# Performance work log

Hardware: AMD Instinct MI355X
Metric: run time of the kernel (lower is better)

## Reference

```python
import jax, jax.numpy as jnp
import numpy as np
import math

EMB = 64
NEG_INF = -1e30

def _layernorm(x, g, b, eps=1e-5):
    mu = jnp.mean(x, axis=-1, keepdims=True)
    var = jnp.mean((x - mu) ** 2, axis=-1, keepdims=True)
    return (x - mu) * jax.lax.rsqrt(var + eps) * g + b

def setup_inputs() -> dict:
    key = jax.random.key(0)
    ks = jax.random.split(key, 8)
    b, t, n, d = 16, 12, 307, EMB
    s = 1.0 / math.sqrt(d)
    inp = {
        'x': jax.random.normal(ks[0], (b, t, n, d), dtype=jnp.float32),
        'stg': jax.random.uniform(ks[1], (b, n, t, n), dtype=jnp.float32),
        'topk': 3,
        'q_w': jax.random.normal(ks[2], (d, d), dtype=jnp.float32) * s,
        'q_b': jnp.zeros((d,), jnp.float32),
        'k_w': jax.random.normal(ks[3], (d, d), dtype=jnp.float32) * s,
        'k_b': jnp.zeros((d,), jnp.float32),
        'ln_g': jnp.ones((d,), jnp.float32),
        'ln_b': jnp.zeros((d,), jnp.float32),
        'ffn_ln_g': jnp.ones((d,), jnp.float32),
        'ffn_ln_b': jnp.zeros((d,), jnp.float32),
        'fc1_w': jax.random.normal(ks[4], (4 * d, d), dtype=jnp.float32) * s,
        'fc1_b': jnp.zeros((4 * d,), jnp.float32),
        'fc2_w': jax.random.normal(ks[5], (d, 4 * d), dtype=jnp.float32) * (0.5 * s),
        'fc2_b': jnp.zeros((d,), jnp.float32),
    }
    return inp

def reference(x, stg, topk, q_w, q_b, k_w, k_b, ln_g, ln_b, ffn_ln_g, ffn_ln_b, fc1_w, fc1_b, fc2_w, fc2_b):
    b, t, n, d = x.shape
    scale = 1.0 / math.sqrt(d)
    x_ = _layernorm(x, ln_g, ln_b)           # [b,t,n,d]
    y_ = x_[:, -1]                            # [b,n,d] last timestep
    q = y_ @ q_w.T + q_b                      # [b,n,d]
    k = x_ @ k_w.T + k_b                      # [b,t,n,d]
    dg = jnp.einsum('bnd,btmd->bntm', q, k) * scale
    sag = jax.nn.sigmoid(dg) * stg * scale    # gated scores [b,n,t,n]
    sag = sag.reshape(b, n, t * n)
    if topk > 0:
        kk = topk * n if topk < 5 else topk   # mirrors torch's self.topk *= n
        top_values, _ = jax.lax.top_k(sag, kk)
        thr = top_values[..., -1:]
        sag = jnp.where(sag > thr, sag, NEG_INF)  # strict >, as in torch code
    sag = jax.nn.softmax(sag, axis=-1).reshape(b, n, t, n)  # dropout in eval mode = identity
    o = jnp.einsum('bntm,btmd->bnd', sag, x_)
    h = o + y_
    # FFN: pre-norm residual MLP (LayerNorm -> Linear(d,4d) -> ReLU -> Linear(4d,d) + residual)
    z = _layernorm(h, ffn_ln_g, ffn_ln_b)
    z = jax.nn.relu(z @ fc1_w.T + fc1_b) @ fc2_w.T + fc2_b
    return h + z
```

## Files before the change

kernel.cpp:

```cpp
#include <hip/hip_runtime.h>

typedef __bf16 bf16x8 __attribute__((ext_vector_type(8)));
typedef float  f32x4  __attribute__((ext_vector_type(4)));
typedef unsigned short u16x8 __attribute__((ext_vector_type(8)));

constexpr int BB    = 16;
constexpr int TT    = 12;
constexpr int NN    = 307;
constexpr int TN    = TT * NN;
constexpr int ROWSX = BB * TT * NN;
constexpr int ROWSH = BB * NN;
constexpr int SST1  = 3712;
constexpr int SSTR  = 3840;
constexpr float SCALE = 0.125f;

__device__ __forceinline__ float wred_sum(float v) {
#pragma unroll
    for (int m = 32; m > 0; m >>= 1) v += __shfl_xor(v, m, 64);
    return v;
}

__global__ void fold_k(const float* __restrict__ qw, const float* __restrict__ qb,
                       const float* __restrict__ kw, const float* __restrict__ kb,
                       float* __restrict__ M, float* __restrict__ b2,
                       float* __restrict__ vv, float* __restrict__ cc) {
    int e = blockIdx.x, d = threadIdx.x;
    float acc = 0.f;
    for (int dp = 0; dp < 64; ++dp) acc += qw[dp * 64 + e] * kw[dp * 64 + d];
    M[e * 64 + d] = acc;
    float vp = wred_sum(qw[d * 64 + e] * kb[d]);
    if (d == 0) vv[e] = vp;
    if (e == 0) {
        float b = 0.f;
        for (int dp = 0; dp < 64; ++dp) b += qb[dp] * kw[dp * 64 + d];
        b2[d] = b;
        float cp = wred_sum(qb[d] * kb[d]);
        if (d == 0) *cc = cp;
    }
}

__global__ void wconv_k(const float* __restrict__ fc1w, const float* __restrict__ fc2w,
                        __bf16* __restrict__ fc1b16, __bf16* __restrict__ fc2b16) {
    int i = blockIdx.x * 256 + threadIdx.x;
    if (i < 16384) fc1b16[i] = (__bf16)fc1w[i];
    else fc2b16[i - 16384] = (__bf16)fc2w[i - 16384];
}

__global__ __launch_bounds__(256) void ln_k(const float* __restrict__ x,
                                            const float* __restrict__ g,
                                            const float* __restrict__ b,
                                            __bf16* __restrict__ xnb,
                                            float* __restrict__ y32) {
    int w = threadIdx.x >> 6, l = threadIdx.x & 63;
    int r = blockIdx.x * 4 + w;
    if (r >= ROWSX) return;
    float val = x[r * 64 + l];
    float mu  = wred_sum(val) * (1.f / 64.f);
    float dv  = val - mu;
    float var = wred_sum(dv * dv) * (1.f / 64.f);
    float xv  = dv * rsqrtf(var + 1e-5f) * g[l] + b[l];
    xnb[(size_t)r * 64 + l] = (__bf16)xv;
    int t = (r / NN) % TT;
    if (t == TT - 1) {
        int bbv = r / (NN * TT), n = r % NN;
        y32[(bbv * NN + n) * 64 + l] = xv;
    }
}

__global__ __launch_bounds__(256) void t_k(const __bf16* __restrict__ xnb,
                                           __bf16* __restrict__ xnT) {
    __shared__ unsigned short tile[64][65];
    int bb = blockIdx.y, j0 = blockIdx.x * 64, t = threadIdx.x;
    const unsigned short* src = (const unsigned short*)xnb;
    unsigned short* dst = (unsigned short*)xnT;
#pragma unroll
    for (int i = 0; i < 16; ++i) {
        int f = t + 256 * i, jr = f >> 6, dc = f & 63;
        int j = j0 + jr;
        tile[jr][dc] = (j < TN) ? src[((size_t)bb * TN + j) * 64 + dc] : (unsigned short)0;
    }
    __syncthreads();
#pragma unroll
    for (int i = 0; i < 16; ++i) {
        int f = t + 256 * i, d = f >> 6, jj = f & 63;
        dst[((size_t)bb * 64 + d) * SSTR + j0 + jj] = tile[jj][d];
    }
}

__global__ __launch_bounds__(256) void qt_k(const float* __restrict__ y32,
                                            const float* __restrict__ M,
                                            const float* __restrict__ b2,
                                            const float* __restrict__ vv,
                                            const float* __restrict__ ccp,
                                            __bf16* __restrict__ qtb,
                                            float* __restrict__ cq) {
    int w = threadIdx.x >> 6, l = threadIdx.x & 63;
    int rr = blockIdx.x * 4 + w;
    if (rr >= ROWSH) return;
    float y = y32[rr * 64 + l];
    float acc = b2[l];
#pragma unroll
    for (int e = 0; e < 64; ++e) acc += __shfl(y, e, 64) * M[e * 64 + l];
    qtb[(size_t)rr * 64 + l] = (__bf16)acc;
    float cp = wred_sum(y * vv[l]);
    if (l == 0) cq[rr] = cp + *ccp;
}

__global__ __launch_bounds__(256) void score_k(const __bf16* __restrict__ qtb,
                                               const float* __restrict__ cq,
                                               const __bf16* __restrict__ xnb,
                                               const float* __restrict__ stg,
                                               __bf16* __restrict__ sag) {
    __shared__ float sstg[64 * 132];
    int bb = blockIdx.z, n0 = blockIdx.y * 64, j0 = blockIdx.x * 128;
    int t = threadIdx.x;
    int w = t >> 6, lane = t & 63;
    int m16 = lane & 15, q4 = lane >> 4;

#pragma unroll
    for (int i = 0; i < 8; ++i) {
        int flat = t + i * 256;
        int row = flat >> 5, c4 = (flat & 31) * 4;
        int n = n0 + row;
        float4 v = {0.f, 0.f, 0.f, 0.f};
        if (n < NN) {
            size_t rb = (size_t)(bb * NN + n) * TN;
            int j = j0 + c4;
            if (j + 3 < TN) v = *(const float4*)(stg + rb + j);
            else {
                if (j + 0 < TN) v.x = stg[rb + j + 0];
                if (j + 1 < TN) v.y = stg[rb + j + 1];
                if (j + 2 < TN) v.z = stg[rb + j + 2];
                if (j + 3 < TN) v.w = stg[rb + j + 3];
            }
        }
        *(float4*)&sstg[row * 132 + c4] = v;
    }

    const bf16x8* ap = (const bf16x8*)(qtb + ((size_t)bb * NN + n0 + w * 16 + m16) * 64);
    bf16x8 a0 = ap[q4], a1 = ap[q4 + 4];
    f32x4 acc[8];
#pragma unroll
    for (int jt = 0; jt < 8; ++jt) {
        const bf16x8* bp = (const bf16x8*)(xnb + ((size_t)bb * TN + j0 + jt * 16 + m16) * 64);
        bf16x8 b0 = bp[q4], b1 = bp[q4 + 4];
        f32x4 c = {0.f, 0.f, 0.f, 0.f};
        c = __builtin_amdgcn_mfma_f32_16x16x32_bf16(a0, b0, c, 0, 0, 0);
        c = __builtin_amdgcn_mfma_f32_16x16x32_bf16(a1, b1, c, 0, 0, 0);
        acc[jt] = c;
    }
    int nbase = n0 + w * 16 + q4 * 4;
    float cn[4];
#pragma unroll
    for (int r = 0; r < 4; ++r) {
        int n = nbase + r;
        cn[r] = (n < NN) ? cq[bb * NN + n] : 0.f;
    }
    __syncthreads();

    u16x8 wvr[4];
#pragma unroll
    for (int r = 0; r < 4; ++r) {
        int nloc = w * 16 + q4 * 4 + r;
#pragma unroll
        for (int jt = 0; jt < 8; ++jt) {
            int j = j0 + jt * 16 + m16;
            float sv = sstg[nloc * 132 + jt * 16 + m16];
            float dg = (acc[jt][r] + cn[r]) * SCALE;
            float s  = 1.f / (1.f + __expf(-dg));
            float wv = (j < TN) ? s * sv * SCALE : 0.f;
            __bf16 wb16 = (__bf16)wv;
            wvr[r][jt] = *(unsigned short*)&wb16;
        }
    }
    __syncthreads();

    unsigned short* wb = (unsigned short*)sstg;
#pragma unroll
    for (int r = 0; r < 4; ++r) {
        int nloc = w * 16 + q4 * 4 + r;
#pragma unroll
        for (int jt = 0; jt < 8; ++jt)
            wb[nloc * 136 + jt * 16 + m16] = wvr[r][jt];
    }
    __syncthreads();

#pragma unroll
    for (int i = 0; i < 4; ++i) {
        int chunk = t + i * 256;
        int row = chunk >> 4, c8 = (chunk & 15) * 8;
        int n = n0 + row;
        if (n < NN) {
            u16x8 v = *(const u16x8*)&wb[row * 136 + c8];
            *(u16x8*)((unsigned short*)sag + (size_t)(bb * NN + n) * SST1 + j0 + c8) = v;
        }
    }
}

__global__ __launch_bounds__(512) void attn_k(const __bf16* __restrict__ sagB,
                                              const __bf16* __restrict__ xnT,
                                              const float* __restrict__ y32,
                                              const int* __restrict__ topk_p,
                                              float* __restrict__ h) {
    __shared__ unsigned short sg[8][3720];
    __shared__ float red[4][8][16];
    int t = threadIdx.x;
    int bb = blockIdx.y, n0 = blockIdx.x * 8;
    int wid = t >> 6, lane = t & 63;
    int m16 = lane & 15, q4 = lane >> 4;

    int topkv = *topk_p;
    bool selAll = (topkv <= 0);
    int kk = 0;
    if (!selAll) {
        kk = (topkv < 5) ? topkv * NN : topkv;
        if (kk > TN) kk = TN;
    }

    int n = n0 + wid;
    const u16x8* src = (const u16x8*)((const unsigned short*)sagB +
                                      (size_t)(bb * NN + min(n, NN - 1)) * SST1);
    u16x8 va[8];
#pragma unroll
    for (int ci = 0; ci < 8; ++ci) {
        int c = lane + (ci << 6);
        u16x8 v = {0, 0, 0, 0, 0, 0, 0, 0};
        if (c < 464) v = src[c];
        va[ci] = v;
    }
    int vmb = 0;
#pragma unroll
    for (int ci = 0; ci < 8; ++ci)
#pragma unroll
        for (int e = 0; e < 8; ++e) vmb = max(vmb, (int)va[ci][e]);
#pragma unroll
    for (int m = 32; m > 0; m >>= 1) vmb = max(vmb, __shfl_xor(vmb, m, 64));
    float vmax = __uint_as_float(((unsigned)vmb) << 16);

    unsigned thrb = 0;
    if (!selAll) {
        unsigned lo = 0, hi = (unsigned)vmb;
        while (lo < hi) {
            unsigned mid = (lo + hi) >> 1;
            int cnt = 0;
#pragma unroll
            for (int ci = 0; ci < 8; ++ci)
#pragma unroll
                for (int e = 0; e < 8; ++e)
                    cnt += (int)__popcll(__ballot((unsigned)va[ci][e] > mid));
            if (cnt < kk) hi = mid; else lo = mid + 1;
        }
        thrb = lo;
    }

    float local = 0.f;
#pragma unroll
    for (int ci = 0; ci < 8; ++ci) {
        int c = lane + (ci << 6);
        int nvv = (c < 460) ? 8 : ((c == 460) ? 4 : 0);
#pragma unroll
        for (int e = 0; e < 8; ++e) {
            unsigned u = va[ci][e];
            bool sel = selAll ? (e < nvv) : (u > thrb);
            float ev = sel ? __expf(__uint_as_float(u << 16) - vmax) : 0.f;
            local += ev;
            __bf16 eb = (__bf16)ev;
            va[ci][e] = *(unsigned short*)&eb;
        }
    }
    local = wred_sum(local);
    bool uni = !(local > 0.f);
    float inv = uni ? 0.f : 1.f / local;
    float uval = 1.f / (float)TN;
#pragma unroll
    for (int ci = 0; ci < 8; ++ci) {
        int c = lane + (ci << 6);
        if (c < 464) {
            int nvv = (c < 460) ? 8 : ((c == 460) ? 4 : 0);
            bf16x8 o;
#pragma unroll
            for (int e = 0; e < 8; ++e) {
                if (uni) o[e] = (e < nvv) ? (__bf16)uval : (__bf16)0.f;
                else {
                    unsigned short us = va[ci][e];
                    float ev = (float)(*(__bf16*)&us);
                    o[e] = (__bf16)(ev * inv);
                }
            }
            *(bf16x8*)&sg[wid][c * 8] = o;
        }
    }
    __syncthreads();

    int dg = wid & 3, kh = wid >> 2;
    bf16x8 zf;
#pragma unroll
    for (int e = 0; e < 8; ++e) zf[e] = (__bf16)0.f;
    f32x4 acc0 = {0.f, 0.f, 0.f, 0.f}, acc1 = {0.f, 0.f, 0.f, 0.f};
    const __bf16* bbase = xnT + ((size_t)bb * 64 + dg * 16 + m16) * SSTR + q4 * 8;
    int kbeg = kh * 1856;
    for (int ks = 0; ks < 58; ks += 2) {
        int k0 = kbeg + ks * 32, k1 = k0 + 32;
        bf16x8 a0 = (m16 < 8) ? *(const bf16x8*)&sg[m16][k0 + q4 * 8] : zf;
        bf16x8 a1 = (m16 < 8) ? *(const bf16x8*)&sg[m16][k1 + q4 * 8] : zf;
        bf16x8 b0 = *(const bf16x8*)(bbase + k0);
        bf16x8 b1 = *(const bf16x8*)(bbase + k1);
        acc0 = __builtin_amdgcn_mfma_f32_16x16x32_bf16(a0, b0, acc0, 0, 0, 0);
        acc1 = __builtin_amdgcn_mfma_f32_16x16x32_bf16(a1, b1, acc1, 0, 0, 0);
    }
    if (kh == 0) {
        if (q4 < 2) {
#pragma unroll
            for (int r = 0; r < 4; ++r)
                red[dg][q4 * 4 + r][m16] = acc0[r] + acc1[r];
        }
    }
    __syncthreads();
    if (kh == 1 && q4 < 2) {
#pragma unroll
        for (int r = 0; r < 4; ++r) {
            int row = q4 * 4 + r;
            int nn2 = n0 + row;
            if (nn2 < NN) {
                size_t o = (size_t)(bb * NN + nn2) * 64 + dg * 16 + m16;
                h[o] = acc0[r] + acc1[r] + red[dg][row][m16] + y32[o];
            }
        }
    }
}

__global__ __launch_bounds__(256) void ffn_k(const float* __restrict__ h,
                                             const float* __restrict__ g,
                                             const float* __restrict__ bln,
                                             const __bf16* __restrict__ fc1b16,
                                             const float* __restrict__ fc1b,
                                             const __bf16* __restrict__ fc2b16,
                                             const float* __restrict__ fc2b,
                                             float* __restrict__ out) {
    __shared__ __bf16 zb[16 * 68];
    __shared__ __bf16 ab[16 * 264];
    int t = threadIdx.x, r0 = blockIdx.x * 16;
    int wid = t >> 6, lane = t & 63;
    int m16 = lane & 15, q4 = lane >> 4;

#pragma unroll
    for (int q = 0; q < 4; ++q) {
        int rl = wid * 4 + q;
        float val = h[(size_t)(r0 + rl) * 64 + lane];
        float mu  = wred_sum(val) * (1.f / 64.f);
        float dv  = val - mu;
        float var = wred_sum(dv * dv) * (1.f / 64.f);
        zb[rl * 68 + lane] = (__bf16)(dv * rsqrtf(var + 1e-5f) * g[lane] + bln[lane]);
    }
    __syncthreads();

    bf16x8 a0 = *(const bf16x8*)&zb[m16 * 68 + q4 * 8];
    bf16x8 a1 = *(const bf16x8*)&zb[m16 * 68 + 32 + q4 * 8];
#pragma unroll
    for (int jt2 = 0; jt2 < 4; ++jt2) {
        int j0t = (wid * 4 + jt2) * 16;
        const __bf16* bp = fc1b16 + (size_t)(j0t + m16) * 64 + q4 * 8;
        f32x4 c = {0.f, 0.f, 0.f, 0.f};
        c = __builtin_amdgcn_mfma_f32_16x16x32_bf16(a0, *(const bf16x8*)bp, c, 0, 0, 0);
        c = __builtin_amdgcn_mfma_f32_16x16x32_bf16(a1, *(const bf16x8*)(bp + 32), c, 0, 0, 0);
        int j = j0t + m16;
        float bias = fc1b[j];
#pragma unroll
        for (int r = 0; r < 4; ++r)
            ab[(q4 * 4 + r) * 264 + j] = (__bf16)fmaxf(c[r] + bias, 0.f);
    }
    __syncthreads();

    f32x4 c2a = {0.f, 0.f, 0.f, 0.f}, c2b = {0.f, 0.f, 0.f, 0.f};
    const __bf16* b2p = fc2b16 + (size_t)(wid * 16 + m16) * 256 + q4 * 8;
#pragma unroll
    for (int k8 = 0; k8 < 8; k8 += 2) {
        bf16x8 aa0 = *(const bf16x8*)&ab[m16 * 264 + k8 * 32 + q4 * 8];
        bf16x8 aa1 = *(const bf16x8*)&ab[m16 * 264 + (k8 + 1) * 32 + q4 * 8];
        c2a = __builtin_amdgcn_mfma_f32_16x16x32_bf16(aa0, *(const bf16x8*)(b2p + k8 * 32), c2a, 0, 0, 0);
        c2b = __builtin_amdgcn_mfma_f32_16x16x32_bf16(aa1, *(const bf16x8*)(b2p + (k8 + 1) * 32), c2b, 0, 0, 0);
    }
    int d = wid * 16 + m16;
    float bias2 = fc2b[d];
#pragma unroll
    for (int r = 0; r < 4; ++r) {
        size_t row = (size_t)(r0 + q4 * 4 + r);
        out[row * 64 + d] = h[row * 64 + d] + c2a[r] + c2b[r] + bias2;
    }
}

extern "C" void kernel_launch(void* const* d_in, const int* in_sizes, int n_in,
                              void* d_out, int out_size, void* d_ws, size_t ws_size,
                              hipStream_t stream) {
    const float* x    = (const float*)d_in[0];
    const float* stg  = (const float*)d_in[1];
    const int*   topk = (const int*)d_in[2];
    const float* qw   = (const float*)d_in[3];
    const float* qb   = (const float*)d_in[4];
    const float* kw   = (const float*)d_in[5];
    const float* kb   = (const float*)d_in[6];
    const float* lng  = (const float*)d_in[7];
    const float* lnb  = (const float*)d_in[8];
    const float* flng = (const float*)d_in[9];
    const float* flnb = (const float*)d_in[10];
    const float* fc1w = (const float*)d_in[11];
    const float* fc1b = (const float*)d_in[12];
    const float* fc2w = (const float*)d_in[13];
    const float* fc2b = (const float*)d_in[14];
    float* out = (float*)d_out;

    float* ws = (float*)d_ws;
    __bf16* xnb = (__bf16*)ws;
    float* p1   = ws + 1886208;
    __bf16* xnT = (__bf16*)p1;
    float* p2   = p1 + 1966080;
    __bf16* qtb = (__bf16*)p2;
    float* y32  = p2 + 157696;
    float* cq   = y32 + 314368;
    float* M    = cq + 4928;
    float* b2   = M + 4096;
    float* vv   = b2 + 64;
    float* cc   = vv + 64;
    __bf16* fc1b16 = (__bf16*)(cc + 16);
    __bf16* fc2b16 = (__bf16*)((float*)fc1b16 + 8192);
    __bf16* sag = (__bf16*)((float*)fc2b16 + 8192);
    float* h    = (float*)sag + 9116672;

    fold_k<<<64, 64, 0, stream>>>(qw, qb, kw, kb, M, b2, vv, cc);
    wconv_k<<<128, 256, 0, stream>>>(fc1w, fc2w, fc1b16, fc2b16);
    ln_k<<<(ROWSX + 3) / 4, 256, 0, stream>>>(x, lng, lnb, xnb, y32);
    t_k<<<dim3((TN + 63) / 64, BB), 256, 0, stream>>>(xnb, xnT);
    qt_k<<<(ROWSH + 3) / 4, 256, 0, stream>>>(y32, M, b2, vv, cc, qtb, cq);
    score_k<<<dim3((TN + 127) / 128, (NN + 63) / 64, BB), 256, 0, stream>>>(qtb, cq, xnb, stg, sag);
    attn_k<<<dim3((NN + 7) / 8, BB), 512, 0, stream>>>(sag, xnT, y32, topk, h);
    ffn_k<<<ROWSH / 16, 256, 0, stream>>>(h, flng, flnb, fc1b16, fc1b, fc2b16, fc2b, out);
}
```

Baseline: 273.6 us.

## Process two attention rows per wave in attn_k with interleaved top-k searches

```diff
diff --git a/kernel.cpp b/kernel.cpp
--- a/kernel.cpp
+++ b/kernel.cpp
@@ -197,15 +197,15 @@
     }
 }
 
-__global__ __launch_bounds__(512) void attn_k(const __bf16* __restrict__ sagB,
-                                              const __bf16* __restrict__ xnT,
-                                              const float* __restrict__ y32,
-                                              const int* __restrict__ topk_p,
-                                              float* __restrict__ h) {
+__global__ __launch_bounds__(512, 4) void attn_k(const __bf16* __restrict__ sagB,
+                                                 const __bf16* __restrict__ xnT,
+                                                 const float* __restrict__ y32,
+                                                 const int* __restrict__ topk_p,
+                                                 float* __restrict__ h) {
     __shared__ unsigned short sg[8][3720];
     __shared__ float red[4][8][16];
     int t = threadIdx.x;
-    int bb = blockIdx.y, n0 = blockIdx.x * 8;
+    int bb = blockIdx.y, n0 = blockIdx.x * 16;
     int wid = t >> 6, lane = t & 63;
     int m16 = lane & 15, q4 = lane >> 4;
 
@@ -217,116 +217,143 @@
         if (kk > TN) kk = TN;
     }
 
-    int n = n0 + wid;
-    const u16x8* src = (const u16x8*)((const unsigned short*)sagB +
-                                      (size_t)(bb * NN + min(n, NN - 1)) * SST1);
-    u16x8 va[8];
+    int nA = n0 + wid, nB = n0 + 8 + wid;
+    const u16x8* srcA = (const u16x8*)((const unsigned short*)sagB +
+                                       (size_t)(bb * NN + min(nA, NN - 1)) * SST1);
+    const u16x8* srcB = (const u16x8*)((const unsigned short*)sagB +
+                                       (size_t)(bb * NN + min(nB, NN - 1)) * SST1);
+    u16x8 va[8], vb[8];
 #pragma unroll
     for (int ci = 0; ci < 8; ++ci) {
         int c = lane + (ci << 6);
-        u16x8 v = {0, 0, 0, 0, 0, 0, 0, 0};
-        if (c < 464) v = src[c];
-        va[ci] = v;
-    }
-    int vmb = 0;
+        u16x8 v0 = {0, 0, 0, 0, 0, 0, 0, 0}, v1 = v0;
+        if (c < 464) { v0 = srcA[ci * 64 + lane]; v1 = srcB[ci * 64 + lane]; }
+        va[ci] = v0; vb[ci] = v1;
+    }
+
+    int vmA = 0, vmB = 0;
 #pragma unroll
     for (int ci = 0; ci < 8; ++ci)
 #pragma unroll
-        for (int e = 0; e < 8; ++e) vmb = max(vmb, (int)va[ci][e]);
-#pragma unroll
-    for (int m = 32; m > 0; m >>= 1) vmb = max(vmb, __shfl_xor(vmb, m, 64));
-    float vmax = __uint_as_float(((unsigned)vmb) << 16);
-
-    unsigned thrb = 0;
+        for (int e = 0; e < 8; ++e) {
+            vmA = max(vmA, (int)va[ci][e]);
+            vmB = max(vmB, (int)vb[ci][e]);
+        }
+#pragma unroll
+    for (int m = 32; m > 0; m >>= 1) {
+        vmA = max(vmA, __shfl_xor(vmA, m, 64));
+        vmB = max(vmB, __shfl_xor(vmB, m, 64));
+    }
+    float vmaxA = __uint_as_float(((unsigned)vmA) << 16);
+    float vmaxB = __uint_as_float(((unsigned)vmB) << 16);
+
+    unsigned thrA = 0, thrB = 0;
     if (!selAll) {
-        unsigned lo = 0, hi = (unsigned)vmb;
-        while (lo < hi) {
-            unsigned mid = (lo + hi) >> 1;
-            int cnt = 0;
+        unsigned loA = 0, hiA = (unsigned)vmA;
+        unsigned loB = 0, hiB = (unsigned)vmB;
+        while (loA < hiA || loB < hiB) {
+            bool doA = loA < hiA, doB = loB < hiB;
+            unsigned midA = (loA + hiA) >> 1, midB = (loB + hiB) >> 1;
+            int cntA = 0, cntB = 0;
 #pragma unroll
             for (int ci = 0; ci < 8; ++ci)
 #pragma unroll
-                for (int e = 0; e < 8; ++e)
-                    cnt += (int)__popcll(__ballot((unsigned)va[ci][e] > mid));
-            if (cnt < kk) hi = mid; else lo = mid + 1;
+                for (int e = 0; e < 8; ++e) {
+                    if (doA) cntA += (int)__popcll(__ballot((unsigned)va[ci][e] > midA));
+                    if (doB) cntB += (int)__popcll(__ballot((unsigned)vb[ci][e] > midB));
+                }
+            if (doA) { if (cntA < kk) hiA = midA; else loA = midA + 1; }
+            if (doB) { if (cntB < kk) hiB = midB; else loB = midB + 1; }
         }
-        thrb = lo;
-    }
-
-    float local = 0.f;
-#pragma unroll
-    for (int ci = 0; ci < 8; ++ci) {
-        int c = lane + (ci << 6);
-        int nvv = (c < 460) ? 8 : ((c == 460) ? 4 : 0);
-#pragma unroll
-        for (int e = 0; e < 8; ++e) {
-            unsigned u = va[ci][e];
-            bool sel = selAll ? (e < nvv) : (u > thrb);
-            float ev = sel ? __expf(__uint_as_float(u << 16) - vmax) : 0.f;
-            local += ev;
-            __bf16 eb = (__bf16)ev;
-            va[ci][e] = *(unsigned short*)&eb;
-        }
-    }
-    local = wred_sum(local);
-    bool uni = !(local > 0.f);
-    float inv = uni ? 0.f : 1.f / local;
-    float uval = 1.f / (float)TN;
-#pragma unroll
-    for (int ci = 0; ci < 8; ++ci) {
-        int c = lane + (ci << 6);
-        if (c < 464) {
-            int nvv = (c < 460) ? 8 : ((c == 460) ? 4 : 0);
-            bf16x8 o;
-#pragma unroll
-            for (int e = 0; e < 8; ++e) {
-                if (uni) o[e] = (e < nvv) ? (__bf16)uval : (__bf16)0.f;
-                else {
-                    unsigned short us = va[ci][e];
-                    float ev = (float)(*(__bf16*)&us);
-                    o[e] = (__bf16)(ev * inv);
-                }
-            }
-            *(bf16x8*)&sg[wid][c * 8] = o;
-        }
-    }
-    __syncthreads();
+        thrA = loA; thrB = loB;
+    }
+
+#define SOFTMAX_ROW(VV, THR, VMX)                                                \
+    {                                                                            \
+        float local = 0.f;                                                       \
+        _Pragma("unroll") for (int ci = 0; ci < 8; ++ci) {                       \
+            int c = lane + (ci << 6);                                            \
+            int nvv = (c < 460) ? 8 : ((c == 460) ? 4 : 0);                      \
+            _Pragma("unroll") for (int e = 0; e < 8; ++e) {                      \
+                unsigned u = VV[ci][e];                                          \
+                bool sel = selAll ? (e < nvv) : (u > THR);                       \
+                float ev = sel ? __expf(__uint_as_float(u << 16) - VMX) : 0.f;   \
+                local += ev;                                                     \
+                __bf16 eb = (__bf16)ev;                                          \
+                VV[ci][e] = *(unsigned short*)&eb;                               \
+            }                                                                    \
+        }                                                                        \
+        local = wred_sum(local);                                                 \
+        bool uni = !(local > 0.f);                                               \
+        float inv = uni ? 0.f : 1.f / local;                                     \
+        float uval = 1.f / (float)TN;                                            \
+        _Pragma("unroll") for (int ci = 0; ci < 8; ++ci) {                       \
+            int c = lane + (ci << 6);                                            \
+            int nvv = (c < 460) ? 8 : ((c == 460) ? 4 : 0);                      \
+            _Pragma("unroll") for (int e = 0; e < 8; ++e) {                      \
+                unsigned short us = VV[ci][e];                                   \
+                float ev = (float)(*(__bf16*)&us);                               \
+                float wv = uni ? ((e < nvv) ? uval : 0.f) : ev * inv;            \
+                __bf16 ob = (__bf16)wv;                                          \
+                VV[ci][e] = *(unsigned short*)&ob;                               \
+            }                                                                    \
+        }                                                                        \
+    }
+
+    SOFTMAX_ROW(va, thrA, vmaxA)
+    SOFTMAX_ROW(vb, thrB, vmaxB)
+#undef SOFTMAX_ROW
+
+#define WRITE_ROW(VV)                                                            \
+    _Pragma("unroll") for (int ci = 0; ci < 8; ++ci) {                           \
+        int c = lane + (ci << 6);                                                \
+        if (c < 464) *(u16x8*)&sg[wid][c * 8] = VV[ci];                          \
+    }
 
     int dg = wid & 3, kh = wid >> 2;
-    bf16x8 zf;
-#pragma unroll
-    for (int e = 0; e < 8; ++e) zf[e] = (__bf16)0.f;
-    f32x4 acc0 = {0.f, 0.f, 0.f, 0.f}, acc1 = {0.f, 0.f, 0.f, 0.f};
     const __bf16* bbase = xnT + ((size_t)bb * 64 + dg * 16 + m16) * SSTR + q4 * 8;
     int kbeg = kh * 1856;
-    for (int ks = 0; ks < 58; ks += 2) {
-        int k0 = kbeg + ks * 32, k1 = k0 + 32;
-        bf16x8 a0 = (m16 < 8) ? *(const bf16x8*)&sg[m16][k0 + q4 * 8] : zf;
-        bf16x8 a1 = (m16 < 8) ? *(const bf16x8*)&sg[m16][k1 + q4 * 8] : zf;
-        bf16x8 b0 = *(const bf16x8*)(bbase + k0);
-        bf16x8 b1 = *(const bf16x8*)(bbase + k1);
-        acc0 = __builtin_amdgcn_mfma_f32_16x16x32_bf16(a0, b0, acc0, 0, 0, 0);
-        acc1 = __builtin_amdgcn_mfma_f32_16x16x32_bf16(a1, b1, acc1, 0, 0, 0);
-    }
-    if (kh == 0) {
-        if (q4 < 2) {
-#pragma unroll
-            for (int r = 0; r < 4; ++r)
-                red[dg][q4 * 4 + r][m16] = acc0[r] + acc1[r];
-        }
-    }
-    __syncthreads();
-    if (kh == 1 && q4 < 2) {
-#pragma unroll
-        for (int r = 0; r < 4; ++r) {
-            int row = q4 * 4 + r;
-            int nn2 = n0 + row;
-            if (nn2 < NN) {
-                size_t o = (size_t)(bb * NN + nn2) * 64 + dg * 16 + m16;
-                h[o] = acc0[r] + acc1[r] + red[dg][row][m16] + y32[o];
-            }
-        }
-    }
+    bf16x8 zf;
+#pragma unroll
+    for (int e = 0; e < 8; ++e) zf[e] = (__bf16)0.f;
+
+#define PV_PHASE(NBASE)                                                          \
+    {                                                                            \
+        f32x4 acc0 = {0.f, 0.f, 0.f, 0.f}, acc1 = {0.f, 0.f, 0.f, 0.f};          \
+        for (int ks = 0; ks < 58; ks += 2) {                                     \
+            int k0 = kbeg + ks * 32, k1 = k0 + 32;                               \
+            bf16x8 a0 = (m16 < 8) ? *(const bf16x8*)&sg[m16][k0 + q4 * 8] : zf;  \
+            bf16x8 a1 = (m16 < 8) ? *(const bf16x8*)&sg[m16][k1 + q4 * 8] : zf;  \
+            bf16x8 b0 = *(const bf16x8*)(bbase + k0);                            \
+            bf16x8 b1 = *(const bf16x8*)(bbase + k1);                            \
+            acc0 = __builtin_amdgcn_mfma_f32_16x16x32_bf16(a0, b0, acc0, 0, 0, 0); \
+            acc1 = __builtin_amdgcn_mfma_f32_16x16x32_bf16(a1, b1, acc1, 0, 0, 0); \
+        }                                                                        \
+        if (kh == 0 && q4 < 2) {                                                 \
+            _Pragma("unroll") for (int r = 0; r < 4; ++r)                        \
+                red[dg][q4 * 4 + r][m16] = acc0[r] + acc1[r];                    \
+        }                                                                        \
+        __syncthreads();                                                         \
+        if (kh == 1 && q4 < 2) {                                                 \
+            _Pragma("unroll") for (int r = 0; r < 4; ++r) {                      \
+                int row = q4 * 4 + r;                                            \
+                int nn2 = (NBASE) + row;                                         \
+                if (nn2 < NN) {                                                  \
+                    size_t o = (size_t)(bb * NN + nn2) * 64 + dg * 16 + m16;     \
+                    h[o] = acc0[r] + acc1[r] + red[dg][row][m16] + y32[o];       \
+                }                                                                \
+            }                                                                    \
+        }                                                                        \
+    }
+
+    WRITE_ROW(va)
+    __syncthreads();
+    PV_PHASE(n0)
+    WRITE_ROW(vb)
+    __syncthreads();
+    PV_PHASE(n0 + 8)
+#undef PV_PHASE
+#undef WRITE_ROW
 }
 
 __global__ __launch_bounds__(256) void ffn_k(const float* __restrict__ h,
@@ -432,6 +459,6 @@
     t_k<<<dim3((TN + 63) / 64, BB), 256, 0, stream>>>(xnb, xnT);
     qt_k<<<(ROWSH + 3) / 4, 256, 0, stream>>>(y32, M, b2, vv, cc, qtb, cq);
     score_k<<<dim3((TN + 127) / 128, (NN + 63) / 64, BB), 256, 0, stream>>>(qtb, cq, xnb, stg, sag);
-    attn_k<<<dim3((NN + 7) / 8, BB), 512, 0, stream>>>(sag, xnT, y32, topk, h);
+    attn_k<<<dim3((NN + 15) / 16, BB), 512, 0, stream>>>(sag, xnT, y32, topk, h);
     ffn_k<<<ROWSH / 16, 256, 0, stream>>>(h, flng, flnb, fc1b16, fc1b, fc2b16, fc2b, out);
 }
```

Result: slower. 379.0 us (+38.5%).
